# Performance work log

Hardware: AMD Instinct MI355X
Metric: run time of the kernel (lower is better)

The kernel has to match this reference:

```python
import jax, jax.numpy as jnp
import numpy as np

N = 20000            # num nodes
E = 320000           # num edges (avg degree 16)
EA = 8               # edge_attr_dim
DIMS = [16, 16, 16]  # layer_sizes
SLOPE = 0.01         # LeakyReLU negative slope


def _leaky(v):
    return jnp.where(v >= 0, v, SLOPE * v)


def setup_inputs() -> dict:
    key = jax.random.key(0)
    ks = jax.random.split(key, 16)
    inp = {
        "x": jax.random.normal(ks[0], (N, DIMS[0]), jnp.float32),
        "edge_index": jax.random.randint(ks[1], (2, E), 0, N),
        "edge_attr": jax.random.normal(ks[2], (E, EA), jnp.float32),
    }
    i = 3
    for l in range(2):
        din, dout = DIMS[l], DIMS[l + 1]
        h = din * dout
        # edge MLP: Linear(EA, h) -> LeakyReLU -> Linear(h, h); second layer small gain (0.01)
        inp[f"w1_{l}"] = jax.random.normal(ks[i], (EA, h), jnp.float32) / np.sqrt(EA); i += 1
        inp[f"b1_{l}"] = jnp.zeros((h,), jnp.float32)
        inp[f"w2_{l}"] = jax.random.normal(ks[i], (h, h), jnp.float32) * (0.01 / np.sqrt(h)); i += 1
        inp[f"b2_{l}"] = jnp.zeros((h,), jnp.float32)
        # NNConv root weight and bias
        inp[f"root_{l}"] = jax.random.normal(ks[i], (din, dout), jnp.float32) / np.sqrt(din); i += 1
        inp[f"bias_{l}"] = jnp.zeros((dout,), jnp.float32)
    return inp


def _nnconv(x, src, dst, edge_attr, w1, b1, w2, b2, root, bias, din, dout):
    # per-edge weight matrix via edge MLP: [E, din*dout] -> [E, din, dout]
    h = _leaky(edge_attr @ w1 + b1)
    W = (h @ w2 + b2).reshape(-1, din, dout)
    # gather source node features, per-edge matmul
    msg = jnp.einsum('ei,eio->eo', x[src], W)          # [E, dout]
    # scatter-mean by destination node
    agg = jax.ops.segment_sum(msg, dst, num_segments=N)
    cnt = jax.ops.segment_sum(jnp.ones((src.shape[0],), x.dtype), dst, num_segments=N)
    mean = agg / jnp.maximum(cnt, 1.0)[:, None]
    # root transform + bias (NNConv defaults: root_weight=True, bias=True)
    return mean + x @ root + bias


def reference(x, edge_index, edge_attr,
              w1_0, b1_0, w2_0, b2_0, root_0, bias_0,
              w1_1, b1_1, w2_1, b2_1, root_1, bias_1):
    src, dst = edge_index[0], edge_index[1]
    h = _nnconv(x, src, dst, edge_attr, w1_0, b1_0, w2_0, b2_0, root_0, bias_0, DIMS[0], DIMS[1])
    h = _leaky(h)  # inter-layer LeakyReLU(0.01); last conv has no activation
    out = _nnconv(h, src, dst, edge_attr, w1_1, b1_1, w2_1, b2_1, root_1, bias_1, DIMS[1], DIMS[2])
    return out
```

## Files before the change

### kernel.cpp

```cpp
#include <hip/hip_runtime.h>

#define NN   20000
#define NE   320000
#define EAD  8
#define DIN  16
#define DOUT 16
#define HH   256
#define SLOPE 0.01f
#define EPB  64
#define MPS  17

typedef __attribute__((ext_vector_type(8))) short bf16x8;
typedef __attribute__((ext_vector_type(4))) float f32x4;

__device__ __forceinline__ float leakyf(float v) { return v >= 0.f ? v : SLOPE * v; }

__device__ __forceinline__ unsigned short f2bf(float f) {
    unsigned int u = __builtin_bit_cast(unsigned int, f);
    u += 0x7FFFu + ((u >> 16) & 1u);
    return (unsigned short)(u >> 16);
}

#define HSWZ(t, idx) ((idx) ^ (((t) & 3) << 4))

__global__ void prep_kernel(const float* __restrict__ w2_0, const float* __restrict__ w2_1,
                            const float* __restrict__ w1_0, const float* __restrict__ w1_1,
                            unsigned short* __restrict__ w2T0, unsigned short* __restrict__ w2T1,
                            unsigned short* __restrict__ w1T0, unsigned short* __restrict__ w1T1)
{
    int idx = blockIdx.x * 256 + threadIdx.x;
    if (idx < HH * HH) {
        int c = idx >> 8, j = idx & 255;
        w2T0[idx] = f2bf(w2_0[j * HH + c]);
        w2T1[idx] = f2bf(w2_1[j * HH + c]);
    }
    if (idx < HH * EAD) {
        int j = idx >> 3, k = idx & 7;
        w1T0[idx] = f2bf(w1_0[k * HH + j]);
        w1T1[idx] = f2bf(w1_1[k * HH + j]);
    }
}

template<int COUNT>
__global__ __launch_bounds__(256, 4)
void edge_kernel(const float* __restrict__ x,
                 const int*   __restrict__ esrc,
                 const int*   __restrict__ edst,
                 const float* __restrict__ ea,
                 const unsigned short* __restrict__ w1T,
                 const float* __restrict__ b1,
                 const unsigned short* __restrict__ w2T,
                 const float* __restrict__ b2,
                 float* __restrict__ agg,
                 float* __restrict__ cnt)
{
    __shared__ __align__(16) unsigned short h_us[EPB * HH];
    __shared__ int ssrc[EPB];
    __shared__ int sdst[EPB];

    const int tid = threadIdx.x;
    const int e0  = blockIdx.x * EPB;
    const int w   = tid >> 6;
    const int ln  = tid & 63;
    const int lo  = ln & 15;
    const int g4  = ln >> 4;

    if (tid < EPB) {
        ssrc[tid] = esrc[e0 + tid];
        sdst[tid] = edst[e0 + tid];
    }

    const unsigned short* bbase = w2T + (size_t)(64 * w + lo) * HH + 8 * g4;
    bf16x8 bcur[4], bnxt[4];
    #pragma unroll
    for (int nt = 0; nt < 4; ++nt) bcur[nt] = *(const bf16x8*)(bbase + nt * 16 * HH);

    bf16x8 zero8;
    #pragma unroll
    for (int k = 0; k < 8; ++k) zero8[k] = 0;

    bf16x8 aW[4], bE[4];
    #pragma unroll
    for (int q = 0; q < 4; ++q) { aW[q] = zero8; bE[q] = zero8; }

    if (ln < 16) {
        #pragma unroll
        for (int jj = 0; jj < 4; ++jj)
            aW[jj] = *(const bf16x8*)(w1T + ((4 * w + jj) * 16 + lo) * EAD);
        #pragma unroll
        for (int tb = 0; tb < 4; ++tb) {
            const float4* p = (const float4*)(ea + (size_t)(e0 + 16 * tb + lo) * EAD);
            float4 a0 = p[0], a1 = p[1];
            bf16x8 v;
            v[0] = (short)f2bf(a0.x); v[1] = (short)f2bf(a0.y);
            v[2] = (short)f2bf(a0.z); v[3] = (short)f2bf(a0.w);
            v[4] = (short)f2bf(a1.x); v[5] = (short)f2bf(a1.y);
            v[6] = (short)f2bf(a1.z); v[7] = (short)f2bf(a1.w);
            bE[tb] = v;
        }
    }

    f32x4 hacc[4][4];
    #pragma unroll
    for (int jj = 0; jj < 4; ++jj) {
        float4 bv = *(const float4*)(b1 + (4 * w + jj) * 16 + 4 * g4);
        f32x4 bi; bi[0] = bv.x; bi[1] = bv.y; bi[2] = bv.z; bi[3] = bv.w;
        #pragma unroll
        for (int tb = 0; tb < 4; ++tb) hacc[jj][tb] = bi;
    }
    #pragma unroll
    for (int jj = 0; jj < 4; ++jj)
        #pragma unroll
        for (int tb = 0; tb < 4; ++tb)
            hacc[jj][tb] = __builtin_amdgcn_mfma_f32_16x16x32_bf16(aW[jj], bE[tb], hacc[jj][tb], 0, 0, 0);

    #pragma unroll
    for (int jj = 0; jj < 4; ++jj) {
        const int j0 = 64 * w + 16 * jj + 4 * g4;
        #pragma unroll
        for (int tb = 0; tb < 4; ++tb) {
            const int t = 16 * tb + lo;
            unsigned int u0 = (unsigned int)f2bf(leakyf(hacc[jj][tb][0]))
                            | ((unsigned int)f2bf(leakyf(hacc[jj][tb][1])) << 16);
            unsigned int u1 = (unsigned int)f2bf(leakyf(hacc[jj][tb][2]))
                            | ((unsigned int)f2bf(leakyf(hacc[jj][tb][3])) << 16);
            uint2 pk; pk.x = u0; pk.y = u1;
            *(uint2*)&h_us[HSWZ(t, t * HH + j0)] = pk;
        }
    }
    __syncthreads();

    f32x4 acc[4][4];
    #pragma unroll
    for (int nt = 0; nt < 4; ++nt) {
        float bv = b2[64 * w + 16 * nt + lo];
        f32x4 bi; bi[0] = bv; bi[1] = bv; bi[2] = bv; bi[3] = bv;
        #pragma unroll
        for (int mt = 0; mt < 4; ++mt) acc[mt][nt] = bi;
    }
    #pragma unroll
    for (int ks = 0; ks < 8; ++ks) {
        if (ks < 7) {
            #pragma unroll
            for (int nt = 0; nt < 4; ++nt)
                bnxt[nt] = *(const bf16x8*)(bbase + nt * 16 * HH + 32 * (ks + 1));
        }
        bf16x8 af[4];
        #pragma unroll
        for (int mt = 0; mt < 4; ++mt) {
            int t = 16 * mt + lo;
            af[mt] = *(const bf16x8*)(h_us + HSWZ(t, t * HH + 32 * ks + 8 * g4));
        }
        #pragma unroll
        for (int mt = 0; mt < 4; ++mt)
            #pragma unroll
            for (int nt = 0; nt < 4; ++nt)
                acc[mt][nt] = __builtin_amdgcn_mfma_f32_16x16x32_bf16(af[mt], bcur[nt], acc[mt][nt], 0, 0, 0);
        #pragma unroll
        for (int nt = 0; nt < 4; ++nt) bcur[nt] = bnxt[nt];
    }
    __syncthreads();

    float* msgp = (float*)h_us;
    #pragma unroll
    for (int mt = 0; mt < 4; ++mt)
        #pragma unroll
        for (int r = 0; r < 4; ++r) {
            const int t = 16 * mt + 4 * g4 + r;
            float4 xv = *(const float4*)(x + (size_t)ssrc[t] * DIN + 4 * w);
            float ps = xv.x * acc[mt][0][r] + xv.y * acc[mt][1][r]
                     + xv.z * acc[mt][2][r] + xv.w * acc[mt][3][r];
            msgp[(w * EPB + t) * MPS + lo] = ps;
        }
    __syncthreads();

    {
        const int t = tid >> 2, p = tid & 3;
        const int d = sdst[t];
        #pragma unroll
        for (int oo = 0; oo < 4; ++oo) {
            const int o = 4 * p + oo;
            float m = msgp[(0 * EPB + t) * MPS + o] + msgp[(1 * EPB + t) * MPS + o]
                    + msgp[(2 * EPB + t) * MPS + o] + msgp[(3 * EPB + t) * MPS + o];
            atomicAdd(&agg[(size_t)d * DOUT + o], m);
        }
        if (COUNT && p == 0) atomicAdd(&cnt[d], 1.0f);
    }
}

__global__ void finalize_kernel(const float* __restrict__ agg,
                                const float* __restrict__ cnt,
                                const float* __restrict__ xin,
                                const float* __restrict__ root,
                                const float* __restrict__ bias,
                                float* __restrict__ out,
                                int do_leaky)
{
    int idx = blockIdx.x * blockDim.x + threadIdx.x;
    if (idx >= NN * DOUT) return;
    int n = idx >> 4, o = idx & 15;
    float c = cnt[n];
    c = c > 1.f ? c : 1.f;
    float v = agg[idx] / c;
    #pragma unroll
    for (int i = 0; i < DIN; ++i)
        v += xin[n * DIN + i] * root[i * DOUT + o];
    v += bias[o];
    out[idx] = do_leaky ? leakyf(v) : v;
}

extern "C" void kernel_launch(void* const* d_in, const int* in_sizes, int n_in,
                              void* d_out, int out_size, void* d_ws, size_t ws_size,
                              hipStream_t stream)
{
    const float* x      = (const float*)d_in[0];
    const int*   ei     = (const int*)  d_in[1];
    const float* ea     = (const float*)d_in[2];
    const float* w1_0   = (const float*)d_in[3];
    const float* b1_0   = (const float*)d_in[4];
    const float* w2_0   = (const float*)d_in[5];
    const float* b2_0   = (const float*)d_in[6];
    const float* root_0 = (const float*)d_in[7];
    const float* bias_0 = (const float*)d_in[8];
    const float* w1_1   = (const float*)d_in[9];
    const float* b1_1   = (const float*)d_in[10];
    const float* w2_1   = (const float*)d_in[11];
    const float* b2_1   = (const float*)d_in[12];
    const float* root_1 = (const float*)d_in[13];
    const float* bias_1 = (const float*)d_in[14];

    const int* esrc = ei;
    const int* edst = ei + NE;

    unsigned short* w2T0 = (unsigned short*)d_ws;
    unsigned short* w2T1 = w2T0 + HH * HH;
    unsigned short* w1T0 = w2T1 + HH * HH;
    unsigned short* w1T1 = w1T0 + HH * EAD;
    float* agg = (float*)(w1T1 + HH * EAD);
    float* cnt = agg + (size_t)NN * DOUT;
    float* x1  = cnt + NN;
    const size_t ws_need = (size_t)((char*)(x1 + (size_t)NN * DIN) - (char*)d_ws);
    if (ws_size < ws_need) return;

    hipMemsetAsync(agg, 0, ((size_t)NN * DOUT + NN) * sizeof(float), stream);
    prep_kernel<<<HH * HH / 256, 256, 0, stream>>>(w2_0, w2_1, w1_0, w1_1,
                                                   w2T0, w2T1, w1T0, w1T1);

    edge_kernel<1><<<NE / EPB, 256, 0, stream>>>(x, esrc, edst, ea,
                                                 w1T0, b1_0, w2T0, b2_0, agg, cnt);
    finalize_kernel<<<(NN * DOUT + 255) / 256, 256, 0, stream>>>(agg, cnt, x,
                                                 root_0, bias_0, x1, 1);
    hipMemsetAsync(agg, 0, (size_t)NN * DOUT * sizeof(float), stream);

    edge_kernel<0><<<NE / EPB, 256, 0, stream>>>(x1, esrc, edst, ea,
                                                 w1T1, b1_1, w2T1, b2_1, agg, cnt);
    finalize_kernel<<<(NN * DOUT + 255) / 256, 256, 0, stream>>>(agg, cnt, x1,
                                                 root_1, bias_1, (float*)d_out, 0);
}
```

Measured before the change: 334.4 us.

## Fold agg zeroing into finalize, packed bf16 converts, raise occupancy bound

Several small changes in one step. The agg buffer is now zeroed inside the first finalize kernel instead of by a separate memset. Float-to-bf16 conversion uses the packed __float22bfloat162_rn intrinsic, and leaky ReLU becomes an fmaxf. The shared src/dst index staging is dropped in favour of direct global loads, and the launch bound rises to 5 blocks per SM. The aim is to cut launch overhead, conversion ALU work and register pressure, at the risk of register spills and redundant global index loads.

```diff
diff --git a/kernel.cpp b/kernel.cpp
--- a/kernel.cpp
+++ b/kernel.cpp
@@ -1,4 +1,5 @@
 #include <hip/hip_runtime.h>
+#include <hip/hip_bf16.h>
 
 #define NN   20000
 #define NE   320000
@@ -13,8 +14,13 @@
 typedef __attribute__((ext_vector_type(8))) short bf16x8;
 typedef __attribute__((ext_vector_type(4))) float f32x4;
 
-__device__ __forceinline__ float leakyf(float v) { return v >= 0.f ? v : SLOPE * v; }
-
+__device__ __forceinline__ float leakyf(float v) { return fmaxf(v, SLOPE * v); }
+
+__device__ __forceinline__ unsigned int pk2bf(float a, float b) {
+    union { __hip_bfloat162 h2; unsigned int u; } cv;
+    cv.h2 = __float22bfloat162_rn(float2{a, b});
+    return cv.u;
+}
 __device__ __forceinline__ unsigned short f2bf(float f) {
     unsigned int u = __builtin_bit_cast(unsigned int, f);
     u += 0x7FFFu + ((u >> 16) & 1u);
@@ -42,7 +48,7 @@
 }
 
 template<int COUNT>
-__global__ __launch_bounds__(256, 4)
+__global__ __launch_bounds__(256, 5)
 void edge_kernel(const float* __restrict__ x,
                  const int*   __restrict__ esrc,
                  const int*   __restrict__ edst,
@@ -55,8 +61,6 @@
                  float* __restrict__ cnt)
 {
     __shared__ __align__(16) unsigned short h_us[EPB * HH];
-    __shared__ int ssrc[EPB];
-    __shared__ int sdst[EPB];
 
     const int tid = threadIdx.x;
     const int e0  = blockIdx.x * EPB;
@@ -65,11 +69,6 @@
     const int lo  = ln & 15;
     const int g4  = ln >> 4;
 
-    if (tid < EPB) {
-        ssrc[tid] = esrc[e0 + tid];
-        sdst[tid] = edst[e0 + tid];
-    }
-
     const unsigned short* bbase = w2T + (size_t)(64 * w + lo) * HH + 8 * g4;
     bf16x8 bcur[4], bnxt[4];
     #pragma unroll
@@ -91,12 +90,12 @@
         for (int tb = 0; tb < 4; ++tb) {
             const float4* p = (const float4*)(ea + (size_t)(e0 + 16 * tb + lo) * EAD);
             float4 a0 = p[0], a1 = p[1];
-            bf16x8 v;
-            v[0] = (short)f2bf(a0.x); v[1] = (short)f2bf(a0.y);
-            v[2] = (short)f2bf(a0.z); v[3] = (short)f2bf(a0.w);
-            v[4] = (short)f2bf(a1.x); v[5] = (short)f2bf(a1.y);
-            v[6] = (short)f2bf(a1.z); v[7] = (short)f2bf(a1.w);
-            bE[tb] = v;
+            union { bf16x8 v8; unsigned int u[4]; } uv;
+            uv.u[0] = pk2bf(a0.x, a0.y);
+            uv.u[1] = pk2bf(a0.z, a0.w);
+            uv.u[2] = pk2bf(a1.x, a1.y);
+            uv.u[3] = pk2bf(a1.z, a1.w);
+            bE[tb] = uv.v8;
         }
     }
 
@@ -120,11 +119,9 @@
         #pragma unroll
         for (int tb = 0; tb < 4; ++tb) {
             const int t = 16 * tb + lo;
-            unsigned int u0 = (unsigned int)f2bf(leakyf(hacc[jj][tb][0]))
-                            | ((unsigned int)f2bf(leakyf(hacc[jj][tb][1])) << 16);
-            unsigned int u1 = (unsigned int)f2bf(leakyf(hacc[jj][tb][2]))
-                            | ((unsigned int)f2bf(leakyf(hacc[jj][tb][3])) << 16);
-            uint2 pk; pk.x = u0; pk.y = u1;
+            uint2 pk;
+            pk.x = pk2bf(leakyf(hacc[jj][tb][0]), leakyf(hacc[jj][tb][1]));
+            pk.y = pk2bf(leakyf(hacc[jj][tb][2]), leakyf(hacc[jj][tb][3]));
             *(uint2*)&h_us[HSWZ(t, t * HH + j0)] = pk;
         }
     }
@@ -167,7 +164,8 @@
         #pragma unroll
         for (int r = 0; r < 4; ++r) {
             const int t = 16 * mt + 4 * g4 + r;
-            float4 xv = *(const float4*)(x + (size_t)ssrc[t] * DIN + 4 * w);
+            const int s = esrc[e0 + t];
+            float4 xv = *(const float4*)(x + (size_t)s * DIN + 4 * w);
             float ps = xv.x * acc[mt][0][r] + xv.y * acc[mt][1][r]
                      + xv.z * acc[mt][2][r] + xv.w * acc[mt][3][r];
             msgp[(w * EPB + t) * MPS + lo] = ps;
@@ -176,7 +174,7 @@
 
     {
         const int t = tid >> 2, p = tid & 3;
-        const int d = sdst[t];
+        const int d = edst[e0 + t];
         #pragma unroll
         for (int oo = 0; oo < 4; ++oo) {
             const int o = 4 * p + oo;
@@ -188,7 +186,8 @@
     }
 }
 
-__global__ void finalize_kernel(const float* __restrict__ agg,
+template<int ZERO>
+__global__ void finalize_kernel(float* __restrict__ agg,
                                 const float* __restrict__ cnt,
                                 const float* __restrict__ xin,
                                 const float* __restrict__ root,
@@ -202,6 +201,7 @@
     float c = cnt[n];
     c = c > 1.f ? c : 1.f;
     float v = agg[idx] / c;
+    if (ZERO) agg[idx] = 0.f;
     #pragma unroll
     for (int i = 0; i < DIN; ++i)
         v += xin[n * DIN + i] * root[i * DOUT + o];
@@ -242,18 +242,16 @@
     const size_t ws_need = (size_t)((char*)(x1 + (size_t)NN * DIN) - (char*)d_ws);
     if (ws_size < ws_need) return;
 
-    hipMemsetAsync(agg, 0, ((size_t)NN * DOUT + NN) * sizeof(float), stream);
+    (void)hipMemsetAsync(agg, 0, ((size_t)NN * DOUT + NN) * sizeof(float), stream);
     prep_kernel<<<HH * HH / 256, 256, 0, stream>>>(w2_0, w2_1, w1_0, w1_1,
                                                    w2T0, w2T1, w1T0, w1T1);
 
     edge_kernel<1><<<NE / EPB, 256, 0, stream>>>(x, esrc, edst, ea,
                                                  w1T0, b1_0, w2T0, b2_0, agg, cnt);
-    finalize_kernel<<<(NN * DOUT + 255) / 256, 256, 0, stream>>>(agg, cnt, x,
+    finalize_kernel<1><<<(NN * DOUT + 255) / 256, 256, 0, stream>>>(agg, cnt, x,
                                                  root_0, bias_0, x1, 1);
-    hipMemsetAsync(agg, 0, (size_t)NN * DOUT * sizeof(float), stream);
-
     edge_kernel<0><<<NE / EPB, 256, 0, stream>>>(x1, esrc, edst, ea,
                                                  w1T1, b1_1, w2T1, b2_1, agg, cnt);
-    finalize_kernel<<<(NN * DOUT + 255) / 256, 256, 0, stream>>>(agg, cnt, x1,
+    finalize_kernel<0><<<(NN * DOUT + 255) / 256, 256, 0, stream>>>(agg, cnt, x1,
                                                  root_1, bias_1, (float*)d_out, 0);
 }
```

Measured after the change: 432.5 us. 1.29x slower.
